# Performance work log

Hardware: AMD Instinct MI355X
Metric: run time of the kernel (lower is better)

The kernel has to match this reference:

```python
import jax, jax.numpy as jnp
import numpy as np

B, S, D, H, HD = 1, 4096, 1024, 16, 64
HALF = HD // 2


def setup_inputs() -> dict:
    key = jax.random.key(0)
    ks = jax.random.split(key, 8)
    std = 0.02
    x = jax.random.normal(ks[0], (B, S, D), dtype=jnp.float32)
    wq_w = jax.random.normal(ks[1], (D, D), dtype=jnp.float32) * std
    wk_w = jax.random.normal(ks[2], (D, D), dtype=jnp.float32) * std
    wv_w = jax.random.normal(ks[3], (D, D), dtype=jnp.float32) * std
    wo_w = jax.random.normal(ks[4], (D, D), dtype=jnp.float32) * std
    wq_b = jnp.zeros((D,), jnp.float32)
    wk_b = jnp.zeros((D,), jnp.float32)
    wv_b = jnp.zeros((D,), jnp.float32)
    wo_b = jnp.zeros((D,), jnp.float32)
    # LLaMA-style rotary frequencies: theta = 10000^{-2i/HD}
    inv_freq = 1.0 / (10000.0 ** (jnp.arange(0, HD, 2, dtype=jnp.float32) / HD))  # [HALF]
    t = jnp.arange(S, dtype=jnp.float32)
    angles = jnp.outer(t, inv_freq)  # [S, HALF]
    freqs_cos = jnp.cos(angles)
    freqs_sin = jnp.sin(angles)
    # causal additive mask (finite large-negative to stay grad-safe)
    mask = jnp.triu(jnp.full((S, S), -1e9, dtype=jnp.float32), k=1)[None, None]
    return {
        "x": x, "start_pos": 0, "freqs_cos": freqs_cos, "freqs_sin": freqs_sin,
        "mask": mask,
        "wq_w": wq_w, "wq_b": wq_b, "wk_w": wk_w, "wk_b": wk_b,
        "wv_w": wv_w, "wv_b": wv_b, "wo_w": wo_w, "wo_b": wo_b,
    }


def _apply_rope(t, cos, sin):
    # t: [B, S, H, HD]; cos/sin: [S, HALF]. Complex multiply on consecutive pairs.
    b, s, h, hd = t.shape
    t2 = t.reshape(b, s, h, hd // 2, 2)
    x0, x1 = t2[..., 0], t2[..., 1]
    c = cos[None, :, None, :]
    sn = sin[None, :, None, :]
    o0 = x0 * c - x1 * sn
    o1 = x0 * sn + x1 * c
    return jnp.stack([o0, o1], axis=-1).reshape(b, s, h, hd)


def reference(x, start_pos, freqs_cos, freqs_sin, mask,
              wq_w, wq_b, wk_w, wk_b, wv_w, wv_b, wo_w, wo_b):
    bsz, seqlen, dim = x.shape
    q = (x @ wq_w.T + wq_b).reshape(bsz, seqlen, H, HD)
    k = (x @ wk_w.T + wk_b).reshape(bsz, seqlen, H, HD)
    v = (x @ wv_w.T + wv_b).reshape(bsz, seqlen, H, HD)
    q = _apply_rope(q, freqs_cos, freqs_sin)
    k = _apply_rope(k, freqs_cos, freqs_sin)
    # [B, H, S, HD]
    q = q.transpose(0, 2, 1, 3)
    k = k.transpose(0, 2, 1, 3)
    v = v.transpose(0, 2, 1, 3)
    scores = jnp.einsum('bhqd,bhkd->bhqk', q, k) / jnp.sqrt(jnp.float32(HD))
    scores = scores + mask
    probs = jax.nn.softmax(scores.astype(jnp.float32), axis=-1).astype(q.dtype)
    out = jnp.einsum('bhqk,bhkd->bhqd', probs, v)  # [B, H, S, HD]
    out = out.transpose(0, 2, 1, 3).reshape(bsz, seqlen, dim)
    return out @ wo_w.T + wo_b
```

## Files before the change

kernel.cpp:

```cpp
#include <hip/hip_runtime.h>


#define S_LEN 4096
#define DIM   1024
#define NH    16
#define HD    64

typedef __attribute__((ext_vector_type(8))) short bf16x8;
typedef __attribute__((ext_vector_type(4))) float f32x4;

__device__ __forceinline__ unsigned short f2b(float f) {
  union { float f; unsigned int u; } v; v.f = f;
  unsigned int r = (v.u + 0x7fffu + ((v.u >> 16) & 1u)) >> 16;
  return (unsigned short)r;
}
__device__ __forceinline__ float b2f(unsigned short h) {
  union { unsigned int u; float f; } v; v.u = ((unsigned int)h) << 16;
  return v.f;
}
__device__ __forceinline__ unsigned int pk2t(float a, float b) {
  union { float f; unsigned int u; } x, y; x.f = a; y.f = b;
  return (x.u >> 16) | (y.u & 0xffff0000u);
}
__device__ __forceinline__ void gload16(const void* g, void* l) {
  __builtin_amdgcn_global_load_lds(
      (const __attribute__((address_space(1))) unsigned int*)g,
      (__attribute__((address_space(3))) unsigned int*)l, 16, 0, 0);
}
__device__ __forceinline__ f32x4 fzero4() { f32x4 z = {0.f, 0.f, 0.f, 0.f}; return z; }

__global__ void cvt_all(const float* __restrict__ x, const float* __restrict__ wq,
                        const float* __restrict__ wk, const float* __restrict__ wv,
                        const float* __restrict__ wo, const float* __restrict__ qb,
                        const float* __restrict__ kb, const float* __restrict__ vbs,
                        const float* __restrict__ ob, unsigned short* __restrict__ xb,
                        unsigned short* __restrict__ wqkvb, unsigned short* __restrict__ wobb,
                        float* __restrict__ biasq, float* __restrict__ biaso) {
  int i = blockIdx.x * 256 + threadIdx.x;
  if (i < 2097152) {
    const float* src; unsigned short* dst; int off;
    if (i < 1048576)      { src = x;  dst = xb;              off = i; }
    else if (i < 1310720) { src = wq; dst = wqkvb;           off = i - 1048576; }
    else if (i < 1572864) { src = wk; dst = wqkvb + 1048576; off = i - 1310720; }
    else if (i < 1835008) { src = wv; dst = wqkvb + 2097152; off = i - 1572864; }
    else                  { src = wo; dst = wobb;            off = i - 1835008; }
    float4 v = ((const float4*)src)[off];
    unsigned int lo = (unsigned int)f2b(v.x) | ((unsigned int)f2b(v.y) << 16);
    unsigned int hi = (unsigned int)f2b(v.z) | ((unsigned int)f2b(v.w) << 16);
    ((uint2*)dst)[off] = make_uint2(lo, hi);
  } else if (i < 2097152 + 1024) {
    int j = i - 2097152;
    if (j < 256)      ((float4*)biasq)[j]              = ((const float4*)qb)[j];
    else if (j < 512) ((float4*)(biasq + 1024))[j-256] = ((const float4*)kb)[j-256];
    else if (j < 768) ((float4*)(biasq + 2048))[j-512] = ((const float4*)vbs)[j-512];
    else              ((float4*)biaso)[j-768]          = ((const float4*)ob)[j-768];
  }
}

__global__ __launch_bounds__(256) void gemm_nt(
    const unsigned short* __restrict__ A, const unsigned short* __restrict__ B,
    const float* __restrict__ bias, float* __restrict__ outF,
    unsigned short* __restrict__ dq, unsigned short* __restrict__ dk,
    unsigned short* __restrict__ dv, int M, int N, int K, int mode) {
  __shared__ alignas(16) unsigned short sA[2][128 * 32];
  __shared__ alignas(16) unsigned short sB[2][128 * 32];
  const int tid = threadIdx.x;
  const int lane = tid & 63, wave = tid >> 6;
  const int ln = lane & 15, quad = lane >> 4;
  const int bm = blockIdx.x * 128, bn = blockIdx.y * 128;
  const int wr = (wave >> 1) * 64, wc = (wave & 1) * 64;

  f32x4 acc[4][4];
#pragma unroll
  for (int i = 0; i < 4; ++i)
#pragma unroll
    for (int j = 0; j < 4; ++j) acc[i][j] = fzero4();

#pragma unroll
  for (int i = 0; i < 2; ++i) {
    int o = (i * 256 + tid) * 16;
    int e = o >> 1;
    int row = e >> 5, col = e & 31;
    gload16(A + (size_t)(bm + row) * K + col, (char*)sA[0] + o);
    gload16(B + (size_t)(bn + row) * K + col, (char*)sB[0] + o);
  }

  int buf = 0;
  for (int k0 = 0; k0 < K; k0 += 32, buf ^= 1) {
    __syncthreads();
    if (k0 + 32 < K) {
#pragma unroll
      for (int i = 0; i < 2; ++i) {
        int o = (i * 256 + tid) * 16;
        int e = o >> 1;
        int row = e >> 5, col = e & 31;
        gload16(A + (size_t)(bm + row) * K + k0 + 32 + col, (char*)sA[buf ^ 1] + o);
        gload16(B + (size_t)(bn + row) * K + k0 + 32 + col, (char*)sB[buf ^ 1] + o);
      }
    }
    bf16x8 af[4], bfr[4];
#pragma unroll
    for (int i = 0; i < 4; ++i) {
      af[i]  = *(const bf16x8*)&sA[buf][(wr + i * 16 + ln) * 32 + quad * 8];
      bfr[i] = *(const bf16x8*)&sB[buf][(wc + i * 16 + ln) * 32 + quad * 8];
    }
#pragma unroll
    for (int i = 0; i < 4; ++i)
#pragma unroll
      for (int j = 0; j < 4; ++j)
        acc[i][j] = __builtin_amdgcn_mfma_f32_16x16x32_bf16(af[i], bfr[j], acc[i][j], 0, 0, 0);
  }

  if (mode == 1) {
#pragma unroll
    for (int i = 0; i < 4; ++i)
#pragma unroll
      for (int j = 0; j < 4; ++j) {
        int n = bn + wc + j * 16 + ln;
        float bi = bias[n];
#pragma unroll
        for (int r = 0; r < 4; ++r) {
          int m = bm + wr + i * 16 + quad * 4 + r;
          outF[(size_t)m * N + n] = acc[i][j][r] + bi;
        }
      }
  } else {
    const int bufi = bn >> 10;
    unsigned short* const base = bufi == 0 ? dq : (bufi == 1 ? dk : dv);
    const int hq = ((bn & 1023) + wc) >> 6;
#pragma unroll
    for (int i = 0; i < 4; ++i)
#pragma unroll
      for (int j = 0; j < 4; ++j) {
        int n = bn + wc + j * 16 + ln;
        float bi = bias[n];
        int hd = j * 16 + ln;
#pragma unroll
        for (int r = 0; r < 4; ++r) {
          int m = bm + wr + i * 16 + quad * 4 + r;
          base[((size_t)(hq * S_LEN + m)) * HD + hd] = f2b(acc[i][j][r] + bi);
        }
      }
  }
}

__global__ void rope_kernel(unsigned short* __restrict__ q, unsigned short* __restrict__ k,
                            const float* __restrict__ fc, const float* __restrict__ fs) {
  int idx = blockIdx.x * 256 + threadIdx.x;
  const int P = NH * S_LEN * 8;
  bool isq = idx < P;
  unsigned short* t = isq ? q : k;
  int i = isq ? idx : idx - P;
  int g = i & 7;
  int s = (i >> 3) & 4095;
  int h = i >> 15;
  const float scale = isq ? 0.180336880f : 1.0f;
  float4 c4 = *(const float4*)&fc[s * 32 + g * 4];
  float4 s4 = *(const float4*)&fs[s * 32 + g * 4];
  uint4* p = (uint4*)&t[((size_t)(h * S_LEN + s)) * HD + g * 8];
  uint4 pv = *p;
  auto rot = [&](unsigned int w, float c, float sn) -> unsigned int {
    float x0 = b2f((unsigned short)(w & 0xffffu));
    float x1 = b2f((unsigned short)(w >> 16));
    float o0 = (x0 * c - x1 * sn) * scale;
    float o1 = (x0 * sn + x1 * c) * scale;
    return (unsigned int)f2b(o0) | ((unsigned int)f2b(o1) << 16);
  };
  pv.x = rot(pv.x, c4.x, s4.x);
  pv.y = rot(pv.y, c4.y, s4.y);
  pv.z = rot(pv.z, c4.z, s4.z);
  pv.w = rot(pv.w, c4.w, s4.w);
  *p = pv;
}

__global__ void transpose_v(const unsigned short* __restrict__ v, unsigned short* __restrict__ vt) {
  __shared__ unsigned short t[64][65];
  const int h = blockIdx.y;
  const int s0 = blockIdx.x * 64;
  const int tid = threadIdx.x;
  const int r = tid >> 2, c0 = (tid & 3) * 16;
  const unsigned short* src = v + ((size_t)h * S_LEN + s0 + r) * HD + c0;
#pragma unroll
  for (int j = 0; j < 16; ++j) t[r][c0 + j] = src[j];
  __syncthreads();
  unsigned short* dst = vt + ((size_t)h * HD + r) * S_LEN + s0 + c0;
#pragma unroll
  for (int j = 0; j < 16; ++j) dst[j] = t[c0 + j][r];
}

__device__ __forceinline__ bf16x8 lds_swzK(const unsigned short* s, int row, int chunk) {
  int byte = row * 128 + ((chunk ^ ((row >> 2) & 7)) << 4);
  return *(const bf16x8*)((const char*)s + byte);
}
__device__ __forceinline__ bf16x8 lds_swzV(const unsigned short* s, int row, int chunk) {
  int byte = row * 128 + ((chunk ^ (row & 7)) << 4);
  return *(const bf16x8*)((const char*)s + byte);
}

__global__ __launch_bounds__(256, 4) void flash_kernel(
    const unsigned short* __restrict__ qg, const unsigned short* __restrict__ kg,
    const unsigned short* __restrict__ vtg, unsigned short* __restrict__ attn) {
  __shared__ alignas(16) unsigned short sK[64 * 64];
  __shared__ alignas(16) unsigned short sV[64 * 64];
  __shared__ alignas(16) unsigned short sP[4 * 16 * 72];

  const int tid = threadIdx.x;
  const int lane = tid & 63, wave = tid >> 6;
  const int ln = lane & 15, quad = lane >> 4;
  const int h = blockIdx.y;
  const int qb = ((h >> 2) & 1) ? (int)blockIdx.x : 63 - (int)blockIdx.x;
  const int q0 = qb * 64;
  const int qrow = q0 + wave * 16;

  const unsigned short* qh = qg + (size_t)h * (S_LEN * HD);
  const unsigned short* kh = kg + (size_t)h * (S_LEN * HD);
  const unsigned short* vh = vtg + (size_t)h * (HD * S_LEN);

  bf16x8 qf[2];
  qf[0] = *(const bf16x8*)(qh + (size_t)(qrow + ln) * HD + quad * 8);
  qf[1] = *(const bf16x8*)(qh + (size_t)(qrow + ln) * HD + 32 + quad * 8);

  f32x4 o_acc[4];
  f32x4 l_acc = fzero4();
#pragma unroll
  for (int t = 0; t < 4; ++t) o_acc[t] = fzero4();
  bf16x8 ones;
#pragma unroll
  for (int j = 0; j < 8; ++j) ones[j] = (short)0x3F80;

  unsigned short* pw = &sP[wave * (16 * 72)];
  const int nkv = qb + 1;

  for (int kt = 0; kt < nkv; ++kt) {
    const int kv0 = kt * 64;
    __syncthreads();
#pragma unroll
    for (int i = 0; i < 2; ++i) {
      int ob = (i * 256 + tid) * 16;
      int row = ob >> 7;
      int ch = (ob >> 4) & 7;
      gload16(kh + (size_t)(kv0 + row) * HD + ((ch ^ ((row >> 2) & 7)) << 3), (char*)sK + ob);
      gload16(vh + (size_t)row * S_LEN + kv0 + ((ch ^ (row & 7)) << 3), (char*)sV + ob);
    }
    __syncthreads();

    f32x4 sc[4];
#pragma unroll
    for (int t = 0; t < 4; ++t) sc[t] = fzero4();
#pragma unroll
    for (int t = 0; t < 4; ++t) {
      int krow = ln * 4 + t;
      bf16x8 kb0 = lds_swzK(sK, krow, quad);
      bf16x8 kb1 = lds_swzK(sK, krow, 4 + quad);
      sc[t] = __builtin_amdgcn_mfma_f32_16x16x32_bf16(qf[0], kb0, sc[t], 0, 0, 0);
      sc[t] = __builtin_amdgcn_mfma_f32_16x16x32_bf16(qf[1], kb1, sc[t], 0, 0, 0);
    }

    if (kt == nkv - 1) {
#pragma unroll
      for (int r = 0; r < 4; ++r) {
        int row = qrow + quad * 4 + r;
        int colb = kv0 + ln * 4;
        float p0 = (colb + 0 <= row) ? __builtin_amdgcn_exp2f(sc[0][r]) : 0.0f;
        float p1 = (colb + 1 <= row) ? __builtin_amdgcn_exp2f(sc[1][r]) : 0.0f;
        float p2 = (colb + 2 <= row) ? __builtin_amdgcn_exp2f(sc[2][r]) : 0.0f;
        float p3 = (colb + 3 <= row) ? __builtin_amdgcn_exp2f(sc[3][r]) : 0.0f;
        *(uint2*)&pw[(quad * 4 + r) * 72 + ln * 4] = make_uint2(pk2t(p0, p1), pk2t(p2, p3));
      }
    } else {
#pragma unroll
      for (int r = 0; r < 4; ++r) {
        float p0 = __builtin_amdgcn_exp2f(sc[0][r]);
        float p1 = __builtin_amdgcn_exp2f(sc[1][r]);
        float p2 = __builtin_amdgcn_exp2f(sc[2][r]);
        float p3 = __builtin_amdgcn_exp2f(sc[3][r]);
        *(uint2*)&pw[(quad * 4 + r) * 72 + ln * 4] = make_uint2(pk2t(p0, p1), pk2t(p2, p3));
      }
    }

    bf16x8 pa0 = *(const bf16x8*)&pw[ln * 72 + quad * 8];
    bf16x8 pa1 = *(const bf16x8*)&pw[ln * 72 + 32 + quad * 8];

    l_acc = __builtin_amdgcn_mfma_f32_16x16x32_bf16(pa0, ones, l_acc, 0, 0, 0);
    l_acc = __builtin_amdgcn_mfma_f32_16x16x32_bf16(pa1, ones, l_acc, 0, 0, 0);

#pragma unroll
    for (int t = 0; t < 4; ++t) {
      int vrow = t * 16 + ln;
      bf16x8 vb0 = lds_swzV(sV, vrow, quad);
      bf16x8 vb1 = lds_swzV(sV, vrow, 4 + quad);
      o_acc[t] = __builtin_amdgcn_mfma_f32_16x16x32_bf16(pa0, vb0, o_acc[t], 0, 0, 0);
      o_acc[t] = __builtin_amdgcn_mfma_f32_16x16x32_bf16(pa1, vb1, o_acc[t], 0, 0, 0);
    }
  }

  float inv[4];
#pragma unroll
  for (int r = 0; r < 4; ++r) inv[r] = 1.0f / l_acc[r];
#pragma unroll
  for (int t = 0; t < 4; ++t)
#pragma unroll
    for (int r = 0; r < 4; ++r) {
      int row = qrow + quad * 4 + r;
      attn[(size_t)row * DIM + h * HD + t * 16 + ln] = f2b(o_acc[t][r] * inv[r]);
    }
}

extern "C" void kernel_launch(void* const* d_in, const int* in_sizes, int n_in,
                              void* d_out, int out_size, void* d_ws, size_t ws_size,
                              hipStream_t stream) {
  const float* x    = (const float*)d_in[0];
  const float* fc   = (const float*)d_in[2];
  const float* fs   = (const float*)d_in[3];
  const float* wqw  = (const float*)d_in[5];
  const float* wqb  = (const float*)d_in[6];
  const float* wkw  = (const float*)d_in[7];
  const float* wkb  = (const float*)d_in[8];
  const float* wvw  = (const float*)d_in[9];
  const float* wvb  = (const float*)d_in[10];
  const float* wow  = (const float*)d_in[11];
  const float* wobf = (const float*)d_in[12];
  float* out = (float*)d_out;

  char* ws = (char*)d_ws;
  const size_t MB = (size_t)1 << 20;
  unsigned short* xb    = (unsigned short*)(ws + 0);
  unsigned short* wqkvb = (unsigned short*)(ws + 8 * MB);
  unsigned short* wobb  = (unsigned short*)(ws + 16 * MB);
  float* biasq = (float*)(ws + 18 * MB);
  float* biaso = (float*)(ws + 18 * MB + 65536);
  unsigned short* qb_ = (unsigned short*)(ws + 19 * MB);
  unsigned short* kb_ = (unsigned short*)(ws + 27 * MB);
  unsigned short* vb_ = (unsigned short*)(ws + 35 * MB);
  unsigned short* vt  = (unsigned short*)(ws + 8 * MB);
  unsigned short* attn = (unsigned short*)(ws + 0);

  cvt_all<<<8196, 256, 0, stream>>>(x, wqw, wkw, wvw, wow, wqb, wkb, wvb, wobf,
                                    xb, wqkvb, wobb, biasq, biaso);
  gemm_nt<<<dim3(32, 24), 256, 0, stream>>>(xb, wqkvb, biasq, nullptr, qb_, kb_, vb_,
                                            4096, 3072, 1024, 0);
  rope_kernel<<<4096, 256, 0, stream>>>(qb_, kb_, fc, fs);
  transpose_v<<<dim3(64, 16), 256, 0, stream>>>(vb_, vt);
  flash_kernel<<<dim3(64, 16), 256, 0, stream>>>(qb_, kb_, vt, attn);
  gemm_nt<<<dim3(32, 8), 256, 0, stream>>>(attn, wobb, biaso, out, nullptr, nullptr, nullptr,
                                           4096, 1024, 1024, 1);
}
```

Before: 281.2 us.

## Fuse RoPE and V transpose into QKV GEMM epilogue; pair causal query blocks

Applies RoPE and the Q scaling inside the QKV GEMM epilogue, using a lane shuffle to fetch each element's pair partner. The V tile is transposed through swizzled LDS and written straight to the transposed layout, so the separate rope and transpose kernels go away along with their global memory round trips. The flash kernel now processes two query blocks per workgroup, blockIdx.x and 63-blockIdx.x, which evens out causal work across a halved grid. The costs are heavier epilogues with per-element cos/sin loads, and fewer workgroups in the attention launch.

```diff
diff --git a/kernel.cpp b/kernel.cpp
--- a/kernel.cpp
+++ b/kernel.cpp
@@ -61,7 +61,8 @@
     const unsigned short* __restrict__ A, const unsigned short* __restrict__ B,
     const float* __restrict__ bias, float* __restrict__ outF,
     unsigned short* __restrict__ dq, unsigned short* __restrict__ dk,
-    unsigned short* __restrict__ dv, int M, int N, int K, int mode) {
+    unsigned short* __restrict__ vtout, const float* __restrict__ fc,
+    const float* __restrict__ fs, int M, int N, int K, int mode) {
   __shared__ alignas(16) unsigned short sA[2][128 * 32];
   __shared__ alignas(16) unsigned short sB[2][128 * 32];
   const int tid = threadIdx.x;
@@ -126,66 +127,58 @@
       }
   } else {
     const int bufi = bn >> 10;
-    unsigned short* const base = bufi == 0 ? dq : (bufi == 1 ? dk : dv);
     const int hq = ((bn & 1023) + wc) >> 6;
-#pragma unroll
-    for (int i = 0; i < 4; ++i)
-#pragma unroll
-      for (int j = 0; j < 4; ++j) {
-        int n = bn + wc + j * 16 + ln;
-        float bi = bias[n];
-        int hd = j * 16 + ln;
-#pragma unroll
-        for (int r = 0; r < 4; ++r) {
-          int m = bm + wr + i * 16 + quad * 4 + r;
-          base[((size_t)(hq * S_LEN + m)) * HD + hd] = f2b(acc[i][j][r] + bi);
-        }
-      }
-  }
-}
-
-__global__ void rope_kernel(unsigned short* __restrict__ q, unsigned short* __restrict__ k,
-                            const float* __restrict__ fc, const float* __restrict__ fs) {
-  int idx = blockIdx.x * 256 + threadIdx.x;
-  const int P = NH * S_LEN * 8;
-  bool isq = idx < P;
-  unsigned short* t = isq ? q : k;
-  int i = isq ? idx : idx - P;
-  int g = i & 7;
-  int s = (i >> 3) & 4095;
-  int h = i >> 15;
-  const float scale = isq ? 0.180336880f : 1.0f;
-  float4 c4 = *(const float4*)&fc[s * 32 + g * 4];
-  float4 s4 = *(const float4*)&fs[s * 32 + g * 4];
-  uint4* p = (uint4*)&t[((size_t)(h * S_LEN + s)) * HD + g * 8];
-  uint4 pv = *p;
-  auto rot = [&](unsigned int w, float c, float sn) -> unsigned int {
-    float x0 = b2f((unsigned short)(w & 0xffffu));
-    float x1 = b2f((unsigned short)(w >> 16));
-    float o0 = (x0 * c - x1 * sn) * scale;
-    float o1 = (x0 * sn + x1 * c) * scale;
-    return (unsigned int)f2b(o0) | ((unsigned int)f2b(o1) << 16);
-  };
-  pv.x = rot(pv.x, c4.x, s4.x);
-  pv.y = rot(pv.y, c4.y, s4.y);
-  pv.z = rot(pv.z, c4.z, s4.z);
-  pv.w = rot(pv.w, c4.w, s4.w);
-  *p = pv;
-}
-
-__global__ void transpose_v(const unsigned short* __restrict__ v, unsigned short* __restrict__ vt) {
-  __shared__ unsigned short t[64][65];
-  const int h = blockIdx.y;
-  const int s0 = blockIdx.x * 64;
-  const int tid = threadIdx.x;
-  const int r = tid >> 2, c0 = (tid & 3) * 16;
-  const unsigned short* src = v + ((size_t)h * S_LEN + s0 + r) * HD + c0;
-#pragma unroll
-  for (int j = 0; j < 16; ++j) t[r][c0 + j] = src[j];
-  __syncthreads();
-  unsigned short* dst = vt + ((size_t)h * HD + r) * S_LEN + s0 + c0;
-#pragma unroll
-  for (int j = 0; j < 16; ++j) dst[j] = t[c0 + j][r];
+    if (bufi < 2) {
+      unsigned short* const base = bufi == 0 ? dq : dk;
+      const float qsc = bufi == 0 ? 0.180336880f : 1.0f;
+#pragma unroll
+      for (int i = 0; i < 4; ++i)
+#pragma unroll
+        for (int j = 0; j < 4; ++j) {
+          int n = bn + wc + j * 16 + ln;
+          float bi = bias[n];
+          int hd = j * 16 + ln;
+          int pi = hd >> 1;
+          bool evn = (ln & 1) == 0;
+#pragma unroll
+          for (int r = 0; r < 4; ++r) {
+            int m = bm + wr + i * 16 + quad * 4 + r;
+            float val = acc[i][j][r] + bi;
+            float par = __shfl_xor(val, 1);
+            float c = fc[m * 32 + pi], sn = fs[m * 32 + pi];
+            float o = evn ? (val * c - par * sn) : (par * sn + val * c);
+            base[((size_t)(hq * S_LEN + m)) * HD + hd] = f2b(o * qsc);
+          }
+        }
+    } else {
+      __syncthreads();
+      unsigned short* scr =
+          (wave < 2 ? (unsigned short*)sA : (unsigned short*)sB) + (wave & 1) * 4096;
+#pragma unroll
+      for (int i = 0; i < 4; ++i)
+#pragma unroll
+        for (int j = 0; j < 4; ++j) {
+          int n = bn + wc + j * 16 + ln;
+          float bi = bias[n];
+          int hd = j * 16 + ln;
+#pragma unroll
+          for (int r = 0; r < 4; ++r) {
+            int sl = i * 16 + quad * 4 + r;
+            int byte = hd * 128 + ((((sl >> 3) ^ (hd & 7)) << 4)) + (sl & 7) * 2;
+            *(unsigned short*)((char*)scr + byte) = f2b(acc[i][j][r] + bi);
+          }
+        }
+#pragma unroll
+      for (int pass = 0; pass < 4; ++pass) {
+        int row = pass * 16 + ln;
+        uint4 d0 = *(uint4*)((char*)scr + row * 128 + (((quad * 2) ^ (row & 7)) << 4));
+        uint4 d1 = *(uint4*)((char*)scr + row * 128 + (((quad * 2 + 1) ^ (row & 7)) << 4));
+        uint4* dst = (uint4*)(vtout + ((size_t)(hq * HD + row)) * S_LEN + bm + wr + quad * 16);
+        dst[0] = d0;
+        dst[1] = d1;
+      }
+    }
+  }
 }
 
 __device__ __forceinline__ bf16x8 lds_swzK(const unsigned short* s, int row, int chunk) {
@@ -208,102 +201,105 @@
   const int lane = tid & 63, wave = tid >> 6;
   const int ln = lane & 15, quad = lane >> 4;
   const int h = blockIdx.y;
-  const int qb = ((h >> 2) & 1) ? (int)blockIdx.x : 63 - (int)blockIdx.x;
-  const int q0 = qb * 64;
-  const int qrow = q0 + wave * 16;
 
   const unsigned short* qh = qg + (size_t)h * (S_LEN * HD);
   const unsigned short* kh = kg + (size_t)h * (S_LEN * HD);
   const unsigned short* vh = vtg + (size_t)h * (HD * S_LEN);
 
-  bf16x8 qf[2];
-  qf[0] = *(const bf16x8*)(qh + (size_t)(qrow + ln) * HD + quad * 8);
-  qf[1] = *(const bf16x8*)(qh + (size_t)(qrow + ln) * HD + 32 + quad * 8);
-
-  f32x4 o_acc[4];
-  f32x4 l_acc = fzero4();
-#pragma unroll
-  for (int t = 0; t < 4; ++t) o_acc[t] = fzero4();
   bf16x8 ones;
 #pragma unroll
   for (int j = 0; j < 8; ++j) ones[j] = (short)0x3F80;
-
   unsigned short* pw = &sP[wave * (16 * 72)];
-  const int nkv = qb + 1;
-
-  for (int kt = 0; kt < nkv; ++kt) {
-    const int kv0 = kt * 64;
-    __syncthreads();
-#pragma unroll
-    for (int i = 0; i < 2; ++i) {
-      int ob = (i * 256 + tid) * 16;
-      int row = ob >> 7;
-      int ch = (ob >> 4) & 7;
-      gload16(kh + (size_t)(kv0 + row) * HD + ((ch ^ ((row >> 2) & 7)) << 3), (char*)sK + ob);
-      gload16(vh + (size_t)row * S_LEN + kv0 + ((ch ^ (row & 7)) << 3), (char*)sV + ob);
+
+  for (int p = 0; p < 2; ++p) {
+    const int qb = p == 0 ? (int)blockIdx.x : 63 - (int)blockIdx.x;
+    const int q0 = qb * 64;
+    const int qrow = q0 + wave * 16;
+
+    bf16x8 qf[2];
+    qf[0] = *(const bf16x8*)(qh + (size_t)(qrow + ln) * HD + quad * 8);
+    qf[1] = *(const bf16x8*)(qh + (size_t)(qrow + ln) * HD + 32 + quad * 8);
+
+    f32x4 o_acc[4];
+    f32x4 l_acc = fzero4();
+#pragma unroll
+    for (int t = 0; t < 4; ++t) o_acc[t] = fzero4();
+
+    const int nkv = qb + 1;
+    for (int kt = 0; kt < nkv; ++kt) {
+      const int kv0 = kt * 64;
+      __syncthreads();
+#pragma unroll
+      for (int i = 0; i < 2; ++i) {
+        int ob = (i * 256 + tid) * 16;
+        int row = ob >> 7;
+        int ch = (ob >> 4) & 7;
+        gload16(kh + (size_t)(kv0 + row) * HD + ((ch ^ ((row >> 2) & 7)) << 3), (char*)sK + ob);
+        gload16(vh + (size_t)row * S_LEN + kv0 + ((ch ^ (row & 7)) << 3), (char*)sV + ob);
+      }
+      __syncthreads();
+
+      f32x4 sc[4];
+#pragma unroll
+      for (int t = 0; t < 4; ++t) sc[t] = fzero4();
+#pragma unroll
+      for (int t = 0; t < 4; ++t) {
+        int krow = ln * 4 + t;
+        bf16x8 kb0 = lds_swzK(sK, krow, quad);
+        bf16x8 kb1 = lds_swzK(sK, krow, 4 + quad);
+        sc[t] = __builtin_amdgcn_mfma_f32_16x16x32_bf16(qf[0], kb0, sc[t], 0, 0, 0);
+        sc[t] = __builtin_amdgcn_mfma_f32_16x16x32_bf16(qf[1], kb1, sc[t], 0, 0, 0);
+      }
+
+      if (kt == nkv - 1) {
+#pragma unroll
+        for (int r = 0; r < 4; ++r) {
+          int row = qrow + quad * 4 + r;
+          int colb = kv0 + ln * 4;
+          float p0 = (colb + 0 <= row) ? __builtin_amdgcn_exp2f(sc[0][r]) : 0.0f;
+          float p1 = (colb + 1 <= row) ? __builtin_amdgcn_exp2f(sc[1][r]) : 0.0f;
+          float p2 = (colb + 2 <= row) ? __builtin_amdgcn_exp2f(sc[2][r]) : 0.0f;
+          float p3 = (colb + 3 <= row) ? __builtin_amdgcn_exp2f(sc[3][r]) : 0.0f;
+          *(uint2*)&pw[(quad * 4 + r) * 72 + ln * 4] = make_uint2(pk2t(p0, p1), pk2t(p2, p3));
+        }
+      } else {
+#pragma unroll
+        for (int r = 0; r < 4; ++r) {
+          float p0 = __builtin_amdgcn_exp2f(sc[0][r]);
+          float p1 = __builtin_amdgcn_exp2f(sc[1][r]);
+          float p2 = __builtin_amdgcn_exp2f(sc[2][r]);
+          float p3 = __builtin_amdgcn_exp2f(sc[3][r]);
+          *(uint2*)&pw[(quad * 4 + r) * 72 + ln * 4] = make_uint2(pk2t(p0, p1), pk2t(p2, p3));
+        }
+      }
+
+      bf16x8 pa0 = *(const bf16x8*)&pw[ln * 72 + quad * 8];
+      bf16x8 pa1 = *(const bf16x8*)&pw[ln * 72 + 32 + quad * 8];
+
+      l_acc = __builtin_amdgcn_mfma_f32_16x16x32_bf16(pa0, ones, l_acc, 0, 0, 0);
+      l_acc = __builtin_amdgcn_mfma_f32_16x16x32_bf16(pa1, ones, l_acc, 0, 0, 0);
+
+#pragma unroll
+      for (int t = 0; t < 4; ++t) {
+        int vrow = t * 16 + ln;
+        bf16x8 vb0 = lds_swzV(sV, vrow, quad);
+        bf16x8 vb1 = lds_swzV(sV, vrow, 4 + quad);
+        o_acc[t] = __builtin_amdgcn_mfma_f32_16x16x32_bf16(pa0, vb0, o_acc[t], 0, 0, 0);
+        o_acc[t] = __builtin_amdgcn_mfma_f32_16x16x32_bf16(pa1, vb1, o_acc[t], 0, 0, 0);
+      }
     }
-    __syncthreads();
-
-    f32x4 sc[4];
-#pragma unroll
-    for (int t = 0; t < 4; ++t) sc[t] = fzero4();
-#pragma unroll
-    for (int t = 0; t < 4; ++t) {
-      int krow = ln * 4 + t;
-      bf16x8 kb0 = lds_swzK(sK, krow, quad);
-      bf16x8 kb1 = lds_swzK(sK, krow, 4 + quad);
-      sc[t] = __builtin_amdgcn_mfma_f32_16x16x32_bf16(qf[0], kb0, sc[t], 0, 0, 0);
-      sc[t] = __builtin_amdgcn_mfma_f32_16x16x32_bf16(qf[1], kb1, sc[t], 0, 0, 0);
-    }
-
-    if (kt == nkv - 1) {
+
+    float inv[4];
+#pragma unroll
+    for (int r = 0; r < 4; ++r) inv[r] = 1.0f / l_acc[r];
+#pragma unroll
+    for (int t = 0; t < 4; ++t)
 #pragma unroll
       for (int r = 0; r < 4; ++r) {
         int row = qrow + quad * 4 + r;
-        int colb = kv0 + ln * 4;
-        float p0 = (colb + 0 <= row) ? __builtin_amdgcn_exp2f(sc[0][r]) : 0.0f;
-        float p1 = (colb + 1 <= row) ? __builtin_amdgcn_exp2f(sc[1][r]) : 0.0f;
-        float p2 = (colb + 2 <= row) ? __builtin_amdgcn_exp2f(sc[2][r]) : 0.0f;
-        float p3 = (colb + 3 <= row) ? __builtin_amdgcn_exp2f(sc[3][r]) : 0.0f;
-        *(uint2*)&pw[(quad * 4 + r) * 72 + ln * 4] = make_uint2(pk2t(p0, p1), pk2t(p2, p3));
-      }
-    } else {
-#pragma unroll
-      for (int r = 0; r < 4; ++r) {
-        float p0 = __builtin_amdgcn_exp2f(sc[0][r]);
-        float p1 = __builtin_amdgcn_exp2f(sc[1][r]);
-        float p2 = __builtin_amdgcn_exp2f(sc[2][r]);
-        float p3 = __builtin_amdgcn_exp2f(sc[3][r]);
-        *(uint2*)&pw[(quad * 4 + r) * 72 + ln * 4] = make_uint2(pk2t(p0, p1), pk2t(p2, p3));
-      }
-    }
-
-    bf16x8 pa0 = *(const bf16x8*)&pw[ln * 72 + quad * 8];
-    bf16x8 pa1 = *(const bf16x8*)&pw[ln * 72 + 32 + quad * 8];
-
-    l_acc = __builtin_amdgcn_mfma_f32_16x16x32_bf16(pa0, ones, l_acc, 0, 0, 0);
-    l_acc = __builtin_amdgcn_mfma_f32_16x16x32_bf16(pa1, ones, l_acc, 0, 0, 0);
-
-#pragma unroll
-    for (int t = 0; t < 4; ++t) {
-      int vrow = t * 16 + ln;
-      bf16x8 vb0 = lds_swzV(sV, vrow, quad);
-      bf16x8 vb1 = lds_swzV(sV, vrow, 4 + quad);
-      o_acc[t] = __builtin_amdgcn_mfma_f32_16x16x32_bf16(pa0, vb0, o_acc[t], 0, 0, 0);
-      o_acc[t] = __builtin_amdgcn_mfma_f32_16x16x32_bf16(pa1, vb1, o_acc[t], 0, 0, 0);
-    }
-  }
-
-  float inv[4];
-#pragma unroll
-  for (int r = 0; r < 4; ++r) inv[r] = 1.0f / l_acc[r];
-#pragma unroll
-  for (int t = 0; t < 4; ++t)
-#pragma unroll
-    for (int r = 0; r < 4; ++r) {
-      int row = qrow + quad * 4 + r;
-      attn[(size_t)row * DIM + h * HD + t * 16 + ln] = f2b(o_acc[t][r] * inv[r]);
-    }
+        attn[(size_t)row * DIM + h * HD + t * 16 + ln] = f2b(o_acc[t][r] * inv[r]);
+      }
+  }
 }
 
 extern "C" void kernel_launch(void* const* d_in, const int* in_sizes, int n_in,
@@ -331,17 +327,14 @@
   float* biaso = (float*)(ws + 18 * MB + 65536);
   unsigned short* qb_ = (unsigned short*)(ws + 19 * MB);
   unsigned short* kb_ = (unsigned short*)(ws + 27 * MB);
-  unsigned short* vb_ = (unsigned short*)(ws + 35 * MB);
-  unsigned short* vt  = (unsigned short*)(ws + 8 * MB);
+  unsigned short* vt  = (unsigned short*)(ws + 35 * MB);
   unsigned short* attn = (unsigned short*)(ws + 0);
 
   cvt_all<<<8196, 256, 0, stream>>>(x, wqw, wkw, wvw, wow, wqb, wkb, wvb, wobf,
                                     xb, wqkvb, wobb, biasq, biaso);
-  gemm_nt<<<dim3(32, 24), 256, 0, stream>>>(xb, wqkvb, biasq, nullptr, qb_, kb_, vb_,
-                                            4096, 3072, 1024, 0);
-  rope_kernel<<<4096, 256, 0, stream>>>(qb_, kb_, fc, fs);
-  transpose_v<<<dim3(64, 16), 256, 0, stream>>>(vb_, vt);
-  flash_kernel<<<dim3(64, 16), 256, 0, stream>>>(qb_, kb_, vt, attn);
+  gemm_nt<<<dim3(32, 24), 256, 0, stream>>>(xb, wqkvb, biasq, nullptr, qb_, kb_, vt,
+                                            fc, fs, 4096, 3072, 1024, 0);
+  flash_kernel<<<dim3(32, 16), 256, 0, stream>>>(qb_, kb_, vt, attn);
   gemm_nt<<<dim3(32, 8), 256, 0, stream>>>(attn, wobb, biaso, out, nullptr, nullptr, nullptr,
-                                           4096, 1024, 1024, 1);
-}
+                                           nullptr, nullptr, 4096, 1024, 1024, 1);
+}
```

Measured after the change: 283.3 us. About the same (+0.8%).
